# Kernel tuning notes

Hardware: AMD Instinct MI355X
Metric: run time of the kernel (lower is better)

## Reference

```python
import jax, jax.numpy as jnp
import numpy as np

BN_EPS = 1e-5

def bn(x, gamma, beta):
    # x: [N, C]; BatchNorm2d over (batch, spatial) == node axis here (training-mode batch stats)
    mu = x.mean(axis=0, keepdims=True)
    var = x.var(axis=0, keepdims=True)
    return (x - mu) * jax.lax.rsqrt(var + BN_EPS) * gamma + beta

def octree_conv(x, neigh, W):
    # x: [N, Cin]; neigh: [N, K] with values in [0, N], N == empty neighbor
    # W: [K, Cin, Cout]. Sparse octree conv = neighbor gather + contraction.
    xp = jnp.concatenate([x, jnp.zeros((1, x.shape[1]), x.dtype)], axis=0)  # zero row for empties
    g = xp[neigh]                                  # [N, K, Cin]
    return jnp.einsum('nkc,kcd->nd', g, W)         # [N, Cout]

def setup_inputs() -> dict:
    key = jax.random.key(0)
    ks = jax.random.split(key, 8)
    N, Cin, Cout, Cb, K = 60000, 256, 512, 128, 27
    s = 0.05
    return {
        'x': jax.random.normal(ks[0], (1, Cin, N, 1), jnp.float32),
        'neigh': jax.random.randint(ks[1], (N, K), 0, N + 1),
        'W1a': jax.random.normal(ks[2], (Cb, Cin), jnp.float32) * s,
        'g1a': jnp.ones((Cb,), jnp.float32), 'b1a': jnp.zeros((Cb,), jnp.float32),
        'W3': jax.random.normal(ks[3], (K, Cb, Cb), jnp.float32) * s,
        'g3': jnp.ones((Cb,), jnp.float32), 'b3': jnp.zeros((Cb,), jnp.float32),
        'W1b': jax.random.normal(ks[4], (Cout, Cb), jnp.float32) * s,
        'g1b': jnp.ones((Cout,), jnp.float32), 'b1b': jnp.zeros((Cout,), jnp.float32),
        'Wc': jax.random.normal(ks[5], (Cout, Cin), jnp.float32) * s,
        'gc': jnp.ones((Cout,), jnp.float32), 'bc': jnp.zeros((Cout,), jnp.float32),
    }

def reference(x, neigh, W1a, g1a, b1a, W3, g3, b3, W1b, g1b, b1b, Wc, gc, bc):
    h = jnp.squeeze(x, axis=(0, 3)).T                         # [N, Cin]
    c1 = jax.nn.relu(bn(h @ W1a.T, g1a, b1a))                 # 1x1 conv + BN + ReLU -> [N, Cb]
    c2 = jax.nn.relu(bn(octree_conv(c1, neigh, W3), g3, b3))  # sparse 3x3 octree conv + BN + ReLU
    c3 = bn(c2 @ W1b.T, g1b, b1b)                             # 1x1 conv + BN -> [N, Cout]
    sc = bn(h @ Wc.T, gc, bc)                                 # shortcut 1x1 conv + BN (Cin != Cout)
    out = jax.nn.relu(c3 + sc)
    return out.T[None, :, :, None]                            # [1, Cout, N, 1]
```

## Files before the change

### kernel.cpp

```cpp
#include <hip/hip_runtime.h>


typedef __bf16 bf16x8 __attribute__((ext_vector_type(8)));
typedef float f32x4 __attribute__((ext_vector_type(4)));
typedef unsigned short u16x8 __attribute__((ext_vector_type(8)));

__device__ __forceinline__ unsigned short f2bfu(float f) {
  union { float f; unsigned u; } v; v.f = f;
  unsigned r = v.u + 0x7fffu + ((v.u >> 16) & 1u);
  return (unsigned short)(r >> 16);
}
__device__ __forceinline__ float bfu2f(unsigned short s) {
  union { unsigned u; float f; } v; v.u = ((unsigned)s) << 16;
  return v.f;
}

__device__ __forceinline__ void gload_lds16(const unsigned short* g, unsigned short* l) {
  __builtin_amdgcn_global_load_lds(
      (const __attribute__((address_space(1))) unsigned int*)(unsigned long long)g,
      (__attribute__((address_space(3))) unsigned int*)(unsigned int)(unsigned long long)l,
      16, 0, 0);
}

__global__ __launch_bounds__(256) void prep_weights(
    const float* __restrict__ W1a, const float* __restrict__ W3,
    const float* __restrict__ W1b, const float* __restrict__ Wc,
    unsigned short* __restrict__ w1a, unsigned short* __restrict__ w3t,
    unsigned short* __restrict__ w1b, unsigned short* __restrict__ wc) {
  int i = blockIdx.x * 256 + threadIdx.x;
  int stride = gridDim.x * 256;
  for (; i < 442368; i += stride) {
    if (i < 32768)  w1a[i] = f2bfu(W1a[i]);
    if (i < 65536)  w1b[i] = f2bfu(W1b[i]);
    if (i < 131072) wc[i]  = f2bfu(Wc[i]);
    int k = i >> 14, rr = i & 16383;
    int d = rr >> 7, c = rr & 127;
    w3t[i] = f2bfu(W3[(k << 14) + (c << 7) + d]);
  }
}

__global__ __launch_bounds__(256) void transpose_x(
    const float* __restrict__ x, unsigned short* __restrict__ h, int M) {
  __shared__ float tile[64][65];
  int n0 = blockIdx.x * 64, c0 = blockIdx.y * 64;
  int t = threadIdx.x;
  int nl = t & 63;
#pragma unroll
  for (int i = 0; i < 16; ++i) {
    int cl = i * 4 + (t >> 6);
    int n = n0 + nl;
    tile[cl][nl] = (n < M) ? x[(size_t)(c0 + cl) * M + n] : 0.f;
  }
  __syncthreads();
  int cl = t & 63;
#pragma unroll
  for (int i = 0; i < 16; ++i) {
    int nl2 = i * 4 + (t >> 6);
    int n = n0 + nl2;
    h[(size_t)n * 256 + c0 + cl] = f2bfu(tile[cl][nl2]);
  }
}

__global__ __launch_bounds__(256) void gemm128(
    const unsigned short* __restrict__ A, const unsigned short* __restrict__ W,
    unsigned short* __restrict__ C, float* __restrict__ partials,
    int M, int Kd, int Nc) {
  __shared__ unsigned short sA[2][128 * 64];
  __shared__ unsigned short sB[2][128 * 64];
  __shared__ float sStat[4][2][128];
  int t = threadIdx.x, wave = t >> 6, lane = t & 63;
  int n0 = blockIdx.x * 128, m0 = blockIdx.y * 128;
  int wr = wave >> 1, wcc = wave & 1;
  int l4 = lane >> 4, lc = lane & 15, lc7 = lc & 7;
  int lrow = lane >> 3, lch = lane & 7;
  f32x4 acc[4][4] = {};
  const int np = Kd >> 6;

  auto STAGE = [&](int p, int buf) {
    int k0 = p << 6;
#pragma unroll
    for (int i = 0; i < 4; ++i) {
      int row = wave * 32 + i * 8 + lrow;
      int sc = lch ^ (row & 7);
      gload_lds16(A + (size_t)(m0 + row) * Kd + k0 + sc * 8, &sA[buf][(wave * 32 + i * 8) * 64]);
    }
#pragma unroll
    for (int i = 0; i < 4; ++i) {
      int row = wave * 32 + i * 8 + lrow;
      int sc = lch ^ (row & 7);
      gload_lds16(W + (size_t)(n0 + row) * Kd + k0 + sc * 8, &sB[buf][(wave * 32 + i * 8) * 64]);
    }
  };
  auto COMPUTE = [&](int buf) {
#pragma unroll
    for (int kk = 0; kk < 2; ++kk) {
      bf16x8 af[4], bfr[4];
#pragma unroll
      for (int mi = 0; mi < 4; ++mi) {
        int row = wr * 64 + mi * 16 + lc;
        int chunk = (kk * 4 + l4) ^ lc7;
        af[mi] = __builtin_bit_cast(bf16x8, *(const u16x8*)(&sA[buf][row * 64 + chunk * 8]));
      }
#pragma unroll
      for (int ni = 0; ni < 4; ++ni) {
        int row = wcc * 64 + ni * 16 + lc;
        int chunk = (kk * 4 + l4) ^ lc7;
        bfr[ni] = __builtin_bit_cast(bf16x8, *(const u16x8*)(&sB[buf][row * 64 + chunk * 8]));
      }
#pragma unroll
      for (int mi = 0; mi < 4; ++mi)
#pragma unroll
        for (int ni = 0; ni < 4; ++ni)
          acc[mi][ni] = __builtin_amdgcn_mfma_f32_16x16x32_bf16(af[mi], bfr[ni], acc[mi][ni], 0, 0, 0);
    }
  };

  STAGE(0, 0);
  __syncthreads();
  int cur = 0;
  for (int p = 0; p < np - 1; ++p) {
    STAGE(p + 1, cur ^ 1);
    COMPUTE(cur);
    __syncthreads();
    cur ^= 1;
  }
  COMPUTE(cur);

#pragma unroll
  for (int ni = 0; ni < 4; ++ni) {
    float s = 0.f, q = 0.f;
    int col = wcc * 64 + ni * 16 + lc;
#pragma unroll
    for (int mi = 0; mi < 4; ++mi)
#pragma unroll
      for (int j = 0; j < 4; ++j) {
        int n = m0 + wr * 64 + mi * 16 + l4 * 4 + j;
        unsigned short u = f2bfu(acc[mi][ni][j]);
        if (n < M) C[(size_t)n * Nc + n0 + col] = u;
        float v = bfu2f(u);
        s += v; q += v * v;
      }
    s += __shfl_xor(s, 16); s += __shfl_xor(s, 32);
    q += __shfl_xor(q, 16); q += __shfl_xor(q, 32);
    if (lane < 16) {
      sStat[wave][0][col] = s;
      sStat[wave][1][col] = q;
    }
  }
  __syncthreads();
  if (t < 128) {
    int wcs = t >> 6;
    float s = sStat[wcs][0][t] + sStat[wcs + 2][0][t];
    float q = sStat[wcs][1][t] + sStat[wcs + 2][1][t];
    partials[(size_t)blockIdx.y * (2 * Nc) + n0 + t] = s;
    partials[(size_t)blockIdx.y * (2 * Nc) + Nc + n0 + t] = q;
  }
}

__global__ __launch_bounds__(512, 4) void octree_gemm(
    const unsigned short* __restrict__ c1, const int* __restrict__ neigh,
    const unsigned short* __restrict__ w3t, unsigned short* __restrict__ c2p,
    float* __restrict__ partials, int M) {
  __shared__ unsigned short sA[2][128 * 64];
  __shared__ unsigned short sB[2][128 * 64];
  __shared__ union {
    unsigned short nidx[128 * 27];
    float stat[8][2][128];
  } u;
  int t = threadIdx.x, wave = t >> 6, lane = t & 63;
  int m0 = blockIdx.x * 128;
  for (int i = t; i < 128 * 27; i += 512) {
    int row = i / 27;
    u.nidx[i] = (unsigned short)((m0 + row < M) ? neigh[(size_t)m0 * 27 + i] : M);
  }
  __syncthreads();

  int wr = wave >> 1, wcc = wave & 1;
  int l4 = lane >> 4, lc = lane & 15, lc7 = lc & 7;
  int lrow = lane >> 3, lch = lane & 7;
  f32x4 acc[2][4] = {};

  auto STAGE = [&](int p, int buf) {
    int k = p >> 1, c0 = (p & 1) << 6;
#pragma unroll
    for (int i = 0; i < 2; ++i) {
      int row = wave * 16 + i * 8 + lrow;
      int nr = u.nidx[row * 27 + k];
      int sc = lch ^ (row & 7);
      gload_lds16(c1 + ((size_t)nr << 7) + c0 + sc * 8, &sA[buf][(wave * 16 + i * 8) * 64]);
    }
    const unsigned short* wk = w3t + ((size_t)k << 14);
#pragma unroll
    for (int i = 0; i < 2; ++i) {
      int row = wave * 16 + i * 8 + lrow;
      int sc = lch ^ (row & 7);
      gload_lds16(wk + ((size_t)row << 7) + c0 + sc * 8, &sB[buf][(wave * 16 + i * 8) * 64]);
    }
  };
  auto COMPUTE = [&](int buf) {
#pragma unroll
    for (int kk = 0; kk < 2; ++kk) {
      bf16x8 af[2], bfr[4];
#pragma unroll
      for (int mi = 0; mi < 2; ++mi) {
        int row = wr * 32 + mi * 16 + lc;
        int chunk = (kk * 4 + l4) ^ lc7;
        af[mi] = __builtin_bit_cast(bf16x8, *(const u16x8*)(&sA[buf][row * 64 + chunk * 8]));
      }
#pragma unroll
      for (int ni = 0; ni < 4; ++ni) {
        int row = wcc * 64 + ni * 16 + lc;
        int chunk = (kk * 4 + l4) ^ lc7;
        bfr[ni] = __builtin_bit_cast(bf16x8, *(const u16x8*)(&sB[buf][row * 64 + chunk * 8]));
      }
      __builtin_amdgcn_s_setprio(1);
#pragma unroll
      for (int mi = 0; mi < 2; ++mi)
#pragma unroll
        for (int ni = 0; ni < 4; ++ni)
          acc[mi][ni] = __builtin_amdgcn_mfma_f32_16x16x32_bf16(af[mi], bfr[ni], acc[mi][ni], 0, 0, 0);
      __builtin_amdgcn_s_setprio(0);
    }
  };

  STAGE(0, 0);
  for (int p = 0; p < 54; ++p) {
    int cur = p & 1;
    if (p < 53) {
      STAGE(p + 1, cur ^ 1);
      asm volatile("s_waitcnt vmcnt(4)" ::: "memory");
    } else {
      asm volatile("s_waitcnt vmcnt(0)" ::: "memory");
    }
    __builtin_amdgcn_sched_barrier(0);
    __builtin_amdgcn_s_barrier();
    __builtin_amdgcn_sched_barrier(0);
    COMPUTE(cur);
    __builtin_amdgcn_sched_barrier(0);
    __builtin_amdgcn_s_barrier();
  }

#pragma unroll
  for (int ni = 0; ni < 4; ++ni) {
    float s = 0.f, q = 0.f;
    int col = wcc * 64 + ni * 16 + lc;
#pragma unroll
    for (int mi = 0; mi < 2; ++mi)
#pragma unroll
      for (int j = 0; j < 4; ++j) {
        int n = m0 + wr * 32 + mi * 16 + l4 * 4 + j;
        unsigned short uo = f2bfu(acc[mi][ni][j]);
        if (n < M) c2p[(size_t)n * 128 + col] = uo;
        float v = bfu2f(uo);
        s += v; q += v * v;
      }
    s += __shfl_xor(s, 16); s += __shfl_xor(s, 32);
    q += __shfl_xor(q, 16); q += __shfl_xor(q, 32);
    if (lane < 16) {
      u.stat[wave][0][col] = s;
      u.stat[wave][1][col] = q;
    }
  }
  __syncthreads();
  if (t < 128) {
    int wcs = t >> 6;
    float s = 0.f, q = 0.f;
#pragma unroll
    for (int g = 0; g < 4; ++g) {
      s += u.stat[g * 2 + wcs][0][t];
      q += u.stat[g * 2 + wcs][1][t];
    }
    partials[(size_t)blockIdx.x * 256 + t] = s;
    partials[(size_t)blockIdx.x * 256 + 128 + t] = q;
  }
}

__global__ __launch_bounds__(256) void bn_finalize(
    const float* __restrict__ partials, int nb, int C, int M,
    const float* __restrict__ g, const float* __restrict__ bt,
    float* __restrict__ ss) {
  int c = blockIdx.x;
  int t = threadIdx.x;
  float s = 0.f, s2 = 0.f;
  for (int b = t; b < nb; b += 256) {
    s += partials[(size_t)b * 2 * C + c];
    s2 += partials[(size_t)b * 2 * C + C + c];
  }
#pragma unroll
  for (int off = 32; off >= 1; off >>= 1) {
    s += __shfl_xor(s, off);
    s2 += __shfl_xor(s2, off);
  }
  __shared__ float sh[4][2];
  int wave = t >> 6, lane = t & 63;
  if (lane == 0) { sh[wave][0] = s; sh[wave][1] = s2; }
  __syncthreads();
  if (t == 0) {
    s = sh[0][0] + sh[1][0] + sh[2][0] + sh[3][0];
    s2 = sh[0][1] + sh[1][1] + sh[2][1] + sh[3][1];
    float mean = s / (float)M;
    float var = s2 / (float)M - mean * mean;
    float sc = g[c] * rsqrtf(var + 1e-5f);
    ss[c] = sc;
    ss[C + c] = bt[c] - mean * sc;
  }
}

__global__ __launch_bounds__(256) void bnrelu(
    const unsigned short* __restrict__ P, const float* __restrict__ ss,
    unsigned short* __restrict__ Aout, int total, int total2, int Cmask) {
  int i = (blockIdx.x * 256 + threadIdx.x) * 8;
  if (i >= total2) return;
  u16x8 o = {0, 0, 0, 0, 0, 0, 0, 0};
  if (i < total) {
    u16x8 v = *(const u16x8*)(P + i);
    int c0 = i & Cmask;
    int C = Cmask + 1;
#pragma unroll
    for (int j = 0; j < 8; ++j) {
      float f = bfu2f(v[j]) * ss[c0 + j] + ss[C + c0 + j];
      o[j] = f2bfu(fmaxf(f, 0.f));
    }
  }
  *(u16x8*)(Aout + i) = o;
}

__global__ __launch_bounds__(256) void final_out(
    const unsigned short* __restrict__ c3p, const unsigned short* __restrict__ scp,
    const float* __restrict__ ss3, const float* __restrict__ sssc,
    float* __restrict__ out, int M) {
  __shared__ float tile[64][65];
  int n0 = blockIdx.x * 64, c0 = blockIdx.y * 64;
  int t = threadIdx.x;
  int cl = t & 63;
#pragma unroll
  for (int i = 0; i < 16; ++i) {
    int nl = i * 4 + (t >> 6);
    int n = n0 + nl;
    float v = 0.f;
    if (n < M) {
      int c = c0 + cl;
      float a = bfu2f(c3p[(size_t)n * 512 + c]) * ss3[c] + ss3[512 + c];
      float b = bfu2f(scp[(size_t)n * 512 + c]) * sssc[c] + sssc[512 + c];
      v = fmaxf(a + b, 0.f);
    }
    tile[nl][cl] = v;
  }
  __syncthreads();
  int nl = t & 63;
#pragma unroll
  for (int i = 0; i < 16; ++i) {
    int cl2 = i * 4 + (t >> 6);
    int n = n0 + nl;
    if (n < M) out[(size_t)(c0 + cl2) * M + n0 + nl] = tile[nl][cl2];
  }
}

extern "C" void kernel_launch(void* const* d_in, const int* in_sizes, int n_in,
                              void* d_out, int out_size, void* d_ws, size_t ws_size,
                              hipStream_t stream) {
  const float* x   = (const float*)d_in[0];
  const int* neigh = (const int*)d_in[1];
  const float* W1a = (const float*)d_in[2];
  const float* g1a = (const float*)d_in[3];
  const float* b1a = (const float*)d_in[4];
  const float* W3  = (const float*)d_in[5];
  const float* g3  = (const float*)d_in[6];
  const float* b3  = (const float*)d_in[7];
  const float* W1b = (const float*)d_in[8];
  const float* g1b = (const float*)d_in[9];
  const float* b1b = (const float*)d_in[10];
  const float* Wc  = (const float*)d_in[11];
  const float* gc  = (const float*)d_in[12];
  const float* bc  = (const float*)d_in[13];
  float* out = (float*)d_out;

  const int M = in_sizes[1] / 27;
  const int MT = (M + 63) / 64;
  const int MTO = (M + 127) / 128;

  char* ws = (char*)d_ws;
  unsigned short* h   = (unsigned short*)(ws + 0);
  unsigned short* wA  = (unsigned short*)(ws + 30736384);
  unsigned short* wP  = (unsigned short*)(ws + 46104576);
  unsigned short* c3p = (unsigned short*)(ws + 61464576);
  unsigned short* scp = (unsigned short*)(ws + 122904576);
  unsigned short* w1a = (unsigned short*)(ws + 184344576);
  unsigned short* w3t = (unsigned short*)(ws + 184410112);
  unsigned short* w1b = (unsigned short*)(ws + 185294848);
  unsigned short* wc  = (unsigned short*)(ws + 185425920);
  float* ss1  = (float*)(ws + 185688064);
  float* ss2  = (float*)(ws + 185692160);
  float* ss3  = (float*)(ws + 185696256);
  float* sssc = (float*)(ws + 185700352);

  float* part12 = (float*)c3p;
  float* part3  = (float*)scp;
  float* partsc = (float*)wP;

  prep_weights<<<1728, 256, 0, stream>>>(W1a, W3, W1b, Wc, w1a, w3t, w1b, wc);
  transpose_x<<<dim3(MT, 4), 256, 0, stream>>>(x, h, M);

  const int total = M * 128, total2 = (MT * 64) * 128;
  const int bnGrid = (total2 / 8 + 255) / 256;

  gemm128<<<dim3(1, MTO), 256, 0, stream>>>(h, w1a, wP, part12, M, 256, 128);
  bn_finalize<<<128, 256, 0, stream>>>(part12, MTO, 128, M, g1a, b1a, ss1);
  bnrelu<<<bnGrid, 256, 0, stream>>>(wP, ss1, wA, total, total2, 127);

  octree_gemm<<<MTO, 512, 0, stream>>>(wA, neigh, w3t, wP, part12, M);
  bn_finalize<<<128, 256, 0, stream>>>(part12, MTO, 128, M, g3, b3, ss2);
  bnrelu<<<bnGrid, 256, 0, stream>>>(wP, ss2, wA, total, total2, 127);

  gemm128<<<dim3(4, MTO), 256, 0, stream>>>(wA, w1b, c3p, part3, M, 128, 512);
  bn_finalize<<<512, 256, 0, stream>>>(part3, MTO, 512, M, g1b, b1b, ss3);

  gemm128<<<dim3(4, MTO), 256, 0, stream>>>(h, wc, scp, partsc, M, 256, 512);
  bn_finalize<<<512, 256, 0, stream>>>(partsc, MTO, 512, M, gc, bc, sssc);

  final_out<<<dim3(MT, 8), 256, 0, stream>>>(c3p, scp, ss3, sssc, out, M);
}
```

Measured before the change: 253.7 us.

## Pipeline gemm128 with explicit vmcnt waits and widen final_out tiles

The gemm128 main loop replaces __syncthreads with explicit s_waitcnt vmcnt plus s_barrier, so the next tile's async LDS loads stay in flight while the current tile is computed. It also raises wave priority around the MFMA block. Separately, final_out now handles 128 channels per block and loads bf16 inputs as 4-wide vectors, halving the grid in the channel dimension. The hand-set vmcnt(8) relies on knowing how many loads STAGE issues, and getting that count wrong could cause a race.

```diff
diff --git a/kernel.cpp b/kernel.cpp
--- a/kernel.cpp
+++ b/kernel.cpp
@@ -4,6 +4,7 @@
 typedef __bf16 bf16x8 __attribute__((ext_vector_type(8)));
 typedef float f32x4 __attribute__((ext_vector_type(4)));
 typedef unsigned short u16x8 __attribute__((ext_vector_type(8)));
+typedef unsigned short u16x4 __attribute__((ext_vector_type(4)));
 
 __device__ __forceinline__ unsigned short f2bfu(float f) {
   union { float f; unsigned u; } v; v.f = f;
@@ -107,24 +108,32 @@
         int chunk = (kk * 4 + l4) ^ lc7;
         bfr[ni] = __builtin_bit_cast(bf16x8, *(const u16x8*)(&sB[buf][row * 64 + chunk * 8]));
       }
+      __builtin_amdgcn_s_setprio(1);
 #pragma unroll
       for (int mi = 0; mi < 4; ++mi)
 #pragma unroll
         for (int ni = 0; ni < 4; ++ni)
           acc[mi][ni] = __builtin_amdgcn_mfma_f32_16x16x32_bf16(af[mi], bfr[ni], acc[mi][ni], 0, 0, 0);
+      __builtin_amdgcn_s_setprio(0);
     }
   };
 
   STAGE(0, 0);
-  __syncthreads();
-  int cur = 0;
-  for (int p = 0; p < np - 1; ++p) {
-    STAGE(p + 1, cur ^ 1);
+  for (int p = 0; p < np; ++p) {
+    int cur = p & 1;
+    if (p < np - 1) {
+      STAGE(p + 1, cur ^ 1);
+      asm volatile("s_waitcnt vmcnt(8)" ::: "memory");
+    } else {
+      asm volatile("s_waitcnt vmcnt(0)" ::: "memory");
+    }
+    __builtin_amdgcn_sched_barrier(0);
+    __builtin_amdgcn_s_barrier();
+    __builtin_amdgcn_sched_barrier(0);
     COMPUTE(cur);
-    __syncthreads();
-    cur ^= 1;
-  }
-  COMPUTE(cur);
+    __builtin_amdgcn_sched_barrier(0);
+    __builtin_amdgcn_s_barrier();
+  }
 
 #pragma unroll
   for (int ni = 0; ni < 4; ++ni) {
@@ -329,30 +338,38 @@
     const unsigned short* __restrict__ c3p, const unsigned short* __restrict__ scp,
     const float* __restrict__ ss3, const float* __restrict__ sssc,
     float* __restrict__ out, int M) {
-  __shared__ float tile[64][65];
-  int n0 = blockIdx.x * 64, c0 = blockIdx.y * 64;
+  __shared__ float tile[64][129];
+  int n0 = blockIdx.x * 64, c0 = blockIdx.y * 128;
   int t = threadIdx.x;
-  int cl = t & 63;
-#pragma unroll
-  for (int i = 0; i < 16; ++i) {
-    int nl = i * 4 + (t >> 6);
+  int rowg = t >> 5, cg = (t & 31) * 4;
+#pragma unroll
+  for (int ps = 0; ps < 8; ++ps) {
+    int nl = ps * 8 + rowg;
     int n = n0 + nl;
-    float v = 0.f;
+    float v0 = 0.f, v1 = 0.f, v2 = 0.f, v3 = 0.f;
     if (n < M) {
-      int c = c0 + cl;
-      float a = bfu2f(c3p[(size_t)n * 512 + c]) * ss3[c] + ss3[512 + c];
-      float b = bfu2f(scp[(size_t)n * 512 + c]) * sssc[c] + sssc[512 + c];
-      v = fmaxf(a + b, 0.f);
-    }
-    tile[nl][cl] = v;
-  }
-  __syncthreads();
-  int nl = t & 63;
-#pragma unroll
-  for (int i = 0; i < 16; ++i) {
-    int cl2 = i * 4 + (t >> 6);
-    int n = n0 + nl;
-    if (n < M) out[(size_t)(c0 + cl2) * M + n0 + nl] = tile[nl][cl2];
+      u16x4 a = *(const u16x4*)(c3p + (size_t)n * 512 + c0 + cg);
+      u16x4 b = *(const u16x4*)(scp + (size_t)n * 512 + c0 + cg);
+      int c = c0 + cg;
+      v0 = fmaxf(bfu2f(a[0]) * ss3[c + 0] + ss3[512 + c + 0] + bfu2f(b[0]) * sssc[c + 0] + sssc[512 + c + 0], 0.f);
+      v1 = fmaxf(bfu2f(a[1]) * ss3[c + 1] + ss3[512 + c + 1] + bfu2f(b[1]) * sssc[c + 1] + sssc[512 + c + 1], 0.f);
+      v2 = fmaxf(bfu2f(a[2]) * ss3[c + 2] + ss3[512 + c + 2] + bfu2f(b[2]) * sssc[c + 2] + sssc[512 + c + 2], 0.f);
+      v3 = fmaxf(bfu2f(a[3]) * ss3[c + 3] + ss3[512 + c + 3] + bfu2f(b[3]) * sssc[c + 3] + sssc[512 + c + 3], 0.f);
+    }
+    tile[nl][cg + 0] = v0;
+    tile[nl][cg + 1] = v1;
+    tile[nl][cg + 2] = v2;
+    tile[nl][cg + 3] = v3;
+  }
+  __syncthreads();
+  int nl = t & 63, cq = t >> 6;
+  int n = n0 + nl;
+  if (n < M) {
+#pragma unroll
+    for (int i = 0; i < 32; ++i) {
+      int cl = i * 4 + cq;
+      out[(size_t)(c0 + cl) * M + n] = tile[nl][cl];
+    }
   }
 }
 
@@ -418,5 +435,5 @@
   gemm128<<<dim3(4, MTO), 256, 0, stream>>>(h, wc, scp, partsc, M, 256, 512);
   bn_finalize<<<512, 256, 0, stream>>>(partsc, MTO, 512, M, gc, bc, sssc);
 
-  final_out<<<dim3(MT, 8), 256, 0, stream>>>(c3p, scp, ss3, sssc, out, M);
-}
+  final_out<<<dim3(MT, 4), 256, 0, stream>>>(c3p, scp, ss3, sssc, out, M);
+}
```

New measurement: 250.2 us. About the same (-1.4%).
